# Optimization experiments

Hardware: AMD Instinct MI355X
Metric: run time of the kernel (lower is better)

The kernel has to match this reference:

```python
import jax, jax.numpy as jnp
import numpy as np

B, L, C = 256, 197, 768
H = C // 16          # reduction = 16
N_ADAPTERS = 10
EPS = 1e-12


def l2_normalize(x, axis=-1):
    sq = jnp.sum(x * x, axis=axis, keepdims=True)
    return x * jax.lax.rsqrt(jnp.maximum(sq, EPS))


def setup_inputs() -> dict:
    key = jax.random.key(0)
    k0, k1, k2, k3 = jax.random.split(key, 4)
    x_embed = jax.random.normal(k0, (B, L, C), dtype=jnp.float32)
    # torch nn.Linear weights are [out_features, in_features]
    W1 = jax.random.normal(k1, (N_ADAPTERS, H, C), dtype=jnp.float32) * 0.02
    W2 = jax.random.normal(k2, (N_ADAPTERS, C, H), dtype=jnp.float32) * 0.02
    adapter_key = jax.random.normal(k3, (N_ADAPTERS, C), dtype=jnp.float32)
    return {"x_embed": x_embed, "W1": W1, "W2": W2, "adapter_key": adapter_key}


def reference(x_embed, W1, W2, adapter_key):
    b = x_embed.shape[0]
    # embedding_key == 'mean'
    x_mean = jnp.mean(x_embed, axis=1)                 # [B, C]
    key_norm = l2_normalize(adapter_key, axis=1)       # [10, C]
    x_norm = l2_normalize(x_mean, axis=1)              # [B, C]
    similarity = x_norm @ key_norm.T                   # [B, 10]

    # top-1 per sample, then majority vote -> single adapter id for the whole batch.
    per_sample_idx = jnp.argmax(similarity, axis=1)    # [B]
    counts = jax.ops.segment_sum(jnp.ones((b,), jnp.float32), per_sample_idx,
                                 num_segments=N_ADAPTERS)
    major = jnp.argmax(counts)                         # ties -> smallest id, matching torch
    idx = jnp.full((b, 1), major, dtype=jnp.int32)     # out['adapter_idx']

    # Apply the selected adapter (same id for every sample); len(idx[i]) == 1.
    w1 = W1[major]                                     # [H, C]
    w2 = W2[major]                                     # [C, H]
    h = jax.nn.relu(jnp.einsum('blc,hc->blh', x_embed, w1))
    a = jax.nn.relu(jnp.einsum('blh,ch->blc', h, w2))
    bias = x_embed + a                                 # (x + adapter(x)) / 1

    adapter_norm = key_norm[idx]                       # [B, 1, C]
    reduce_sim = jnp.sum(adapter_norm * x_norm[:, None, :]) / b
    return bias, reduce_sim, idx
```

## Files before the change

### kernel.cpp

```cpp
#include <hip/hip_runtime.h>
#include <hip/hip_bf16.h>

#define B_   256
#define L_   197
#define C_   768
#define H_   48
#define NA_  10
#define ROWS (B_ * L_)
#define TR   16
#define XP   772
#define HP   72
#define NBLK (ROWS / TR)
#define OFF_SIM 38731776
#define OFF_IDX 38731777

typedef __attribute__((ext_vector_type(8))) short short8;
typedef __attribute__((ext_vector_type(4))) short short4_t;
typedef __attribute__((ext_vector_type(4))) float f32x4;

static __device__ inline short f2bf(float f) {
    union { float f; unsigned u; } v; v.f = f;
    unsigned r = v.u + 0x7fffu + ((v.u >> 16) & 1u);
    return (short)(r >> 16);
}

#define GL2LDS(g, l) __builtin_amdgcn_global_load_lds( \
    (const __attribute__((address_space(1))) void*)(g), \
    (__attribute__((address_space(3))) void*)(l), 16, 0, 0)

#define GLW(dst, p, OFF) asm volatile("global_load_dwordx4 %0, %1, off offset:" OFF \
    : "=v"(dst) : "v"(p))

__global__ void kw_convert(const float* __restrict__ W1, const float* __restrict__ W2,
                           short* __restrict__ W1b, short* __restrict__ W2b) {
    int i = blockIdx.x * 256 + threadIdx.x;
    if (i < NA_ * H_ * C_)
        W1b[i] = f2bf(W1[i]);
    if (i < NA_ * C_ * 64) {
        int k  = i & 63;
        int nc = i >> 6;
        W2b[i] = (k < H_) ? f2bf(W2[nc * H_ + k]) : (short)0;
    }
}

__global__ void k1a_partial(const float* __restrict__ x, float* __restrict__ partial) {
    int b = blockIdx.x >> 2, seg = blockIdx.x & 3;
    int l0 = seg * 50, l1 = l0 + 50; if (l1 > L_) l1 = L_;
    int t = threadIdx.x;
    const float* xb = x + (size_t)b * L_ * C_ + t * 4;
    float4 s = {0.f, 0.f, 0.f, 0.f};
    #pragma unroll 5
    for (int l = l0; l < l1; ++l) {
        float4 v = *(const float4*)(xb + (size_t)l * C_);
        s.x += v.x; s.y += v.y; s.z += v.z; s.w += v.w;
    }
    *(float4*)(partial + ((size_t)b * 4 + seg) * C_ + t * 4) = s;
}

__global__ void k1b_sims(const float* __restrict__ partial, const float* __restrict__ akey,
                         float* __restrict__ sims) {
    __shared__ float red[21][256];
    int b = blockIdx.x, t = threadIdx.x;
    const float* p = partial + (size_t)b * 4 * C_;
    float m[3];
    #pragma unroll
    for (int j = 0; j < 3; ++j) {
        int c = t + j * 256;
        m[j] = (p[c] + p[C_ + c] + p[2 * C_ + c] + p[3 * C_ + c]) * (1.f / (float)L_);
    }
    red[0][t] = m[0] * m[0] + m[1] * m[1] + m[2] * m[2];
    #pragma unroll
    for (int k = 0; k < NA_; ++k) {
        float kd = 0.f, kq = 0.f;
        #pragma unroll
        for (int j = 0; j < 3; ++j) {
            float kv = akey[k * C_ + t + j * 256];
            kd += m[j] * kv; kq += kv * kv;
        }
        red[1 + k][t] = kd; red[11 + k][t] = kq;
    }
    __syncthreads();
    for (int s = 128; s > 0; s >>= 1) {
        if (t < s) {
            #pragma unroll
            for (int q = 0; q < 21; ++q) red[q][t] += red[q][t + s];
        }
        __syncthreads();
    }
    if (t < NA_) {
        float msq = red[0][0];
        sims[b * NA_ + t] = red[1 + t][0] * rsqrtf(fmaxf(red[11 + t][0], 1e-12f))
                                          * rsqrtf(fmaxf(msq, 1e-12f));
    }
}

__global__ void k2_select(const float* __restrict__ sims, float* __restrict__ out,
                          int* __restrict__ majorp) {
    __shared__ int counts[NA_];
    __shared__ int majorS;
    __shared__ float rs[256];
    int t = threadIdx.x;
    float s[NA_];
    #pragma unroll
    for (int k = 0; k < NA_; ++k) s[k] = sims[t * NA_ + k];
    int best = 0; float bv = s[0];
    #pragma unroll
    for (int k = 1; k < NA_; ++k) { if (s[k] > bv) { bv = s[k]; best = k; } }
    if (t < NA_) counts[t] = 0;
    __syncthreads();
    atomicAdd(&counts[best], 1);
    __syncthreads();
    if (t == 0) {
        int mj = 0, mc = counts[0];
        #pragma unroll
        for (int k = 1; k < NA_; ++k) { if (counts[k] > mc) { mc = counts[k]; mj = k; } }
        majorS = mj; *majorp = mj;
    }
    __syncthreads();
    int mj = majorS;
    rs[t] = s[mj];
    __syncthreads();
    for (int st = 128; st > 0; st >>= 1) { if (t < st) rs[t] += rs[t + st]; __syncthreads(); }
    if (t == 0) out[OFF_SIM] = rs[0] * (1.f / (float)B_);
    out[OFF_IDX + t] = (float)mj;
}

__launch_bounds__(192, 2)
__global__ void k3_apply(const float* __restrict__ x, const short* __restrict__ W1b,
                         const short* __restrict__ W2b, const int* __restrict__ majorp,
                         float* __restrict__ out) {
    __shared__ float xs[TR * XP];
    __shared__ short hs[TR * HP];
    const int major = *majorp;

    int t = threadIdx.x;
    int w = t >> 6, l = t & 63;
    int rbase = blockIdx.x * TR;
    int lo16 = l & 15;
    int g = l >> 4;
    int klane = g * 8;

    {
        const float* xsrc = x + (size_t)rbase * C_ + w * 256 + l * 4;
        #pragma unroll
        for (int i = 0; i < TR; ++i)
            GL2LDS(xsrc + (size_t)i * C_, &xs[i * XP + w * 256]);
    }
    __syncthreads();

    {
        const short* w1p = W1b + major * (H_ * C_) + (size_t)(w * 16 + lo16) * C_ + klane;
        f32x4 acc = {0, 0, 0, 0};
        short8 q0, q1, q2, q3, q4, q5, q6, q7, q8, q9, q10, q11;

#define G1STEP(KK, Q) { \
        const int k0 = (KK) * 32; \
        f32x4 xa = *(const f32x4*)&xs[lo16 * XP + k0 + klane]; \
        f32x4 xb = *(const f32x4*)&xs[lo16 * XP + k0 + klane + 4]; \
        short8 af; \
        af[0] = f2bf(xa[0]); af[1] = f2bf(xa[1]); af[2] = f2bf(xa[2]); af[3] = f2bf(xa[3]); \
        af[4] = f2bf(xb[0]); af[5] = f2bf(xb[1]); af[6] = f2bf(xb[2]); af[7] = f2bf(xb[3]); \
        acc = __builtin_amdgcn_mfma_f32_16x16x32_bf16(af, Q, acc, 0, 0, 0); }

        GLW(q0, w1p, "0");    GLW(q1, w1p, "64");   GLW(q2, w1p, "128");
        GLW(q3, w1p, "192");  GLW(q4, w1p, "256");  GLW(q5, w1p, "320");
        GLW(q6, w1p, "384");  GLW(q7, w1p, "448");  GLW(q8, w1p, "512");
        GLW(q9, w1p, "576");  GLW(q10, w1p, "640"); GLW(q11, w1p, "704");
        asm volatile("s_waitcnt vmcnt(0)"
            : "+v"(q0), "+v"(q1), "+v"(q2), "+v"(q3), "+v"(q4), "+v"(q5),
              "+v"(q6), "+v"(q7), "+v"(q8), "+v"(q9), "+v"(q10), "+v"(q11));
        __builtin_amdgcn_sched_barrier(0);
        G1STEP(0, q0)  G1STEP(1, q1)  G1STEP(2, q2)  G1STEP(3, q3)
        G1STEP(4, q4)  G1STEP(5, q5)  G1STEP(6, q6)  G1STEP(7, q7)
        G1STEP(8, q8)  G1STEP(9, q9)  G1STEP(10, q10) G1STEP(11, q11)

        GLW(q0, w1p, "768");  GLW(q1, w1p, "832");  GLW(q2, w1p, "896");
        GLW(q3, w1p, "960");  GLW(q4, w1p, "1024"); GLW(q5, w1p, "1088");
        GLW(q6, w1p, "1152"); GLW(q7, w1p, "1216"); GLW(q8, w1p, "1280");
        GLW(q9, w1p, "1344"); GLW(q10, w1p, "1408"); GLW(q11, w1p, "1472");
        asm volatile("s_waitcnt vmcnt(0)"
            : "+v"(q0), "+v"(q1), "+v"(q2), "+v"(q3), "+v"(q4), "+v"(q5),
              "+v"(q6), "+v"(q7), "+v"(q8), "+v"(q9), "+v"(q10), "+v"(q11));
        __builtin_amdgcn_sched_barrier(0);
        G1STEP(12, q0) G1STEP(13, q1) G1STEP(14, q2) G1STEP(15, q3)
        G1STEP(16, q4) G1STEP(17, q5) G1STEP(18, q6) G1STEP(19, q7)
        G1STEP(20, q8) G1STEP(21, q9) G1STEP(22, q10) G1STEP(23, q11)
#undef G1STEP

        #pragma unroll
        for (int q = 0; q < 4; ++q)
            hs[(g * 4 + q) * HP + w * 16 + lo16] = f2bf(fmaxf(acc[q], 0.f));
        if (w == 0) {
            short4_t z = {0, 0, 0, 0};
            *(short4_t*)&hs[lo16 * HP + 48 + g * 4] = z;
        }
    }
    __syncthreads();

    {
        short8 hA = *(const short8*)&hs[lo16 * HP + klane];
        short8 hB = *(const short8*)&hs[lo16 * HP + 32 + klane];
        const short* w2base = W2b + (size_t)major * (C_ * 64) + lo16 * 64 + klane;

        #pragma unroll
        for (int b = 0; b < 4; ++b) {
            const int j0 = b * 4;
            const short* pa = w2base + (size_t)(w * 16 + j0) * 1024;
            const short* pb = pa + 2048;
            short8 r00, r01, r10, r11, r20, r21, r30, r31;
            GLW(r00, pa, "0");    GLW(r01, pa, "64");
            GLW(r10, pa, "2048"); GLW(r11, pa, "2112");
            GLW(r20, pb, "0");    GLW(r21, pb, "64");
            GLW(r30, pb, "2048"); GLW(r31, pb, "2112");
            asm volatile("s_waitcnt vmcnt(0)"
                : "+v"(r00), "+v"(r01), "+v"(r10), "+v"(r11),
                  "+v"(r20), "+v"(r21), "+v"(r30), "+v"(r31));
            __builtin_amdgcn_sched_barrier(0);

#define G2STEP(JJ, P0, P1) { \
            const int it = w * 16 + j0 + (JJ); \
            f32x4 acc = {0, 0, 0, 0}; \
            acc = __builtin_amdgcn_mfma_f32_16x16x32_bf16(P0, hA, acc, 0, 0, 0); \
            acc = __builtin_amdgcn_mfma_f32_16x16x32_bf16(P1, hB, acc, 0, 0, 0); \
            float* xp = &xs[lo16 * XP + it * 16 + g * 4]; \
            f32x4 xv = *(const f32x4*)xp; \
            f32x4 ov; \
            ov[0] = xv[0] + fmaxf(acc[0], 0.f); \
            ov[1] = xv[1] + fmaxf(acc[1], 0.f); \
            ov[2] = xv[2] + fmaxf(acc[2], 0.f); \
            ov[3] = xv[3] + fmaxf(acc[3], 0.f); \
            *(f32x4*)xp = ov; }

            G2STEP(0, r00, r01) G2STEP(1, r10, r11)
            G2STEP(2, r20, r21) G2STEP(3, r30, r31)
#undef G2STEP
        }
    }
    __syncthreads();

    {
        float* od = out + (size_t)rbase * C_ + t * 4;
        #pragma unroll
        for (int row = 0; row < TR; ++row) {
            f32x4 v = *(const f32x4*)&xs[row * XP + t * 4];
            *(f32x4*)(od + (size_t)row * C_) = v;
        }
    }
}

extern "C" void kernel_launch(void* const* d_in, const int* in_sizes, int n_in,
                              void* d_out, int out_size, void* d_ws, size_t ws_size,
                              hipStream_t stream) {
    const float* x    = (const float*)d_in[0];
    const float* W1   = (const float*)d_in[1];
    const float* W2   = (const float*)d_in[2];
    const float* akey = (const float*)d_in[3];
    float* out = (float*)d_out;

    char* ws = (char*)d_ws;
    short* W1b     = (short*)ws;
    short* W2b     = (short*)(ws + 737280);
    float* partial = (float*)(ws + 1720320);
    float* sims    = (float*)(ws + 4866048);
    int*   majorp  = (int*)(ws + 4876288);

    hipLaunchKernelGGL(kw_convert, dim3(1920), dim3(256), 0, stream, W1, W2, W1b, W2b);
    hipLaunchKernelGGL(k1a_partial, dim3(B_ * 4), dim3(192), 0, stream, x, partial);
    hipLaunchKernelGGL(k1b_sims, dim3(B_), dim3(256), 0, stream, partial, akey, sims);
    hipLaunchKernelGGL(k2_select, dim3(1), dim3(256), 0, stream, sims, out, majorp);
    hipLaunchKernelGGL(k3_apply, dim3(NBLK), dim3(192), 0, stream, x, W1b, W2b, majorp, out);
}
```

Measured before the change: 128.6 us.

## Prefetch all adapter weights up front and write outputs directly from registers

Issues all 24 W1 loads at once and waits on partial vmcnt counts, so the second half of the loads overlaps the first half of the MFMAs. W2 loads are likewise issued all at once, consumed in two waves, and the epilogue writes results straight to global memory. This removes the LDS round trip, the final barrier and the separate copy-out loop, and bf16 conversion now uses the HIP intrinsic. It raises register pressure, which may lower occupancy, and the direct stores are 16-byte scattered writes per lane rather than fully coalesced rows.

New measurement: 129.5 us. No clear change (+0.7%).

```diff
diff --git a/kernel.cpp b/kernel.cpp
--- a/kernel.cpp
+++ b/kernel.cpp
@@ -23,6 +23,11 @@
     unsigned r = v.u + 0x7fffu + ((v.u >> 16) & 1u);
     return (short)(r >> 16);
 }
+static __device__ inline short bfc(float f) {
+    __hip_bfloat16 h = __float2bfloat16(f);
+    union { __hip_bfloat16 h; short s; } u; u.h = h;
+    return u.s;
+}
 
 #define GL2LDS(g, l) __builtin_amdgcn_global_load_lds( \
     (const __attribute__((address_space(1))) void*)(g), \
@@ -152,44 +157,44 @@
         const short* w1p = W1b + major * (H_ * C_) + (size_t)(w * 16 + lo16) * C_ + klane;
         f32x4 acc = {0, 0, 0, 0};
         short8 q0, q1, q2, q3, q4, q5, q6, q7, q8, q9, q10, q11;
+        short8 q12, q13, q14, q15, q16, q17, q18, q19, q20, q21, q22, q23;
 
 #define G1STEP(KK, Q) { \
         const int k0 = (KK) * 32; \
         f32x4 xa = *(const f32x4*)&xs[lo16 * XP + k0 + klane]; \
         f32x4 xb = *(const f32x4*)&xs[lo16 * XP + k0 + klane + 4]; \
         short8 af; \
-        af[0] = f2bf(xa[0]); af[1] = f2bf(xa[1]); af[2] = f2bf(xa[2]); af[3] = f2bf(xa[3]); \
-        af[4] = f2bf(xb[0]); af[5] = f2bf(xb[1]); af[6] = f2bf(xb[2]); af[7] = f2bf(xb[3]); \
+        af[0] = bfc(xa[0]); af[1] = bfc(xa[1]); af[2] = bfc(xa[2]); af[3] = bfc(xa[3]); \
+        af[4] = bfc(xb[0]); af[5] = bfc(xb[1]); af[6] = bfc(xb[2]); af[7] = bfc(xb[3]); \
         acc = __builtin_amdgcn_mfma_f32_16x16x32_bf16(af, Q, acc, 0, 0, 0); }
 
-        GLW(q0, w1p, "0");    GLW(q1, w1p, "64");   GLW(q2, w1p, "128");
-        GLW(q3, w1p, "192");  GLW(q4, w1p, "256");  GLW(q5, w1p, "320");
-        GLW(q6, w1p, "384");  GLW(q7, w1p, "448");  GLW(q8, w1p, "512");
-        GLW(q9, w1p, "576");  GLW(q10, w1p, "640"); GLW(q11, w1p, "704");
-        asm volatile("s_waitcnt vmcnt(0)"
+        GLW(q0,  w1p, "0");    GLW(q1,  w1p, "64");   GLW(q2,  w1p, "128");
+        GLW(q3,  w1p, "192");  GLW(q4,  w1p, "256");  GLW(q5,  w1p, "320");
+        GLW(q6,  w1p, "384");  GLW(q7,  w1p, "448");  GLW(q8,  w1p, "512");
+        GLW(q9,  w1p, "576");  GLW(q10, w1p, "640");  GLW(q11, w1p, "704");
+        GLW(q12, w1p, "768");  GLW(q13, w1p, "832");  GLW(q14, w1p, "896");
+        GLW(q15, w1p, "960");  GLW(q16, w1p, "1024"); GLW(q17, w1p, "1088");
+        GLW(q18, w1p, "1152"); GLW(q19, w1p, "1216"); GLW(q20, w1p, "1280");
+        GLW(q21, w1p, "1344"); GLW(q22, w1p, "1408"); GLW(q23, w1p, "1472");
+        asm volatile("s_waitcnt vmcnt(12)"
             : "+v"(q0), "+v"(q1), "+v"(q2), "+v"(q3), "+v"(q4), "+v"(q5),
               "+v"(q6), "+v"(q7), "+v"(q8), "+v"(q9), "+v"(q10), "+v"(q11));
         __builtin_amdgcn_sched_barrier(0);
         G1STEP(0, q0)  G1STEP(1, q1)  G1STEP(2, q2)  G1STEP(3, q3)
         G1STEP(4, q4)  G1STEP(5, q5)  G1STEP(6, q6)  G1STEP(7, q7)
         G1STEP(8, q8)  G1STEP(9, q9)  G1STEP(10, q10) G1STEP(11, q11)
-
-        GLW(q0, w1p, "768");  GLW(q1, w1p, "832");  GLW(q2, w1p, "896");
-        GLW(q3, w1p, "960");  GLW(q4, w1p, "1024"); GLW(q5, w1p, "1088");
-        GLW(q6, w1p, "1152"); GLW(q7, w1p, "1216"); GLW(q8, w1p, "1280");
-        GLW(q9, w1p, "1344"); GLW(q10, w1p, "1408"); GLW(q11, w1p, "1472");
         asm volatile("s_waitcnt vmcnt(0)"
-            : "+v"(q0), "+v"(q1), "+v"(q2), "+v"(q3), "+v"(q4), "+v"(q5),
-              "+v"(q6), "+v"(q7), "+v"(q8), "+v"(q9), "+v"(q10), "+v"(q11));
-        __builtin_amdgcn_sched_barrier(0);
-        G1STEP(12, q0) G1STEP(13, q1) G1STEP(14, q2) G1STEP(15, q3)
-        G1STEP(16, q4) G1STEP(17, q5) G1STEP(18, q6) G1STEP(19, q7)
-        G1STEP(20, q8) G1STEP(21, q9) G1STEP(22, q10) G1STEP(23, q11)
+            : "+v"(q12), "+v"(q13), "+v"(q14), "+v"(q15), "+v"(q16), "+v"(q17),
+              "+v"(q18), "+v"(q19), "+v"(q20), "+v"(q21), "+v"(q22), "+v"(q23));
+        __builtin_amdgcn_sched_barrier(0);
+        G1STEP(12, q12) G1STEP(13, q13) G1STEP(14, q14) G1STEP(15, q15)
+        G1STEP(16, q16) G1STEP(17, q17) G1STEP(18, q18) G1STEP(19, q19)
+        G1STEP(20, q20) G1STEP(21, q21) G1STEP(22, q22) G1STEP(23, q23)
 #undef G1STEP
 
         #pragma unroll
         for (int q = 0; q < 4; ++q)
-            hs[(g * 4 + q) * HP + w * 16 + lo16] = f2bf(fmaxf(acc[q], 0.f));
+            hs[(g * 4 + q) * HP + w * 16 + lo16] = bfc(fmaxf(acc[q], 0.f));
         if (w == 0) {
             short4_t z = {0, 0, 0, 0};
             *(short4_t*)&hs[lo16 * HP + 48 + g * 4] = z;
@@ -200,51 +205,72 @@
     {
         short8 hA = *(const short8*)&hs[lo16 * HP + klane];
         short8 hB = *(const short8*)&hs[lo16 * HP + 32 + klane];
-        const short* w2base = W2b + (size_t)major * (C_ * 64) + lo16 * 64 + klane;
-
-        #pragma unroll
-        for (int b = 0; b < 4; ++b) {
-            const int j0 = b * 4;
-            const short* pa = w2base + (size_t)(w * 16 + j0) * 1024;
-            const short* pb = pa + 2048;
-            short8 r00, r01, r10, r11, r20, r21, r30, r31;
-            GLW(r00, pa, "0");    GLW(r01, pa, "64");
-            GLW(r10, pa, "2048"); GLW(r11, pa, "2112");
-            GLW(r20, pb, "0");    GLW(r21, pb, "64");
-            GLW(r30, pb, "2048"); GLW(r31, pb, "2112");
-            asm volatile("s_waitcnt vmcnt(0)"
-                : "+v"(r00), "+v"(r01), "+v"(r10), "+v"(r11),
-                  "+v"(r20), "+v"(r21), "+v"(r30), "+v"(r31));
-            __builtin_amdgcn_sched_barrier(0);
+        const short* ba = W2b + (size_t)major * (C_ * 64)
+                              + (size_t)(w * 16) * 1024 + lo16 * 64 + klane;
+        const short* b1 = ba + 2048;
+        const short* b2 = ba + 4096;
+        const short* b3 = ba + 6144;
+        const short* b4 = ba + 8192;
+        const short* b5 = ba + 10240;
+        const short* b6 = ba + 12288;
+        const short* b7 = ba + 14336;
+        short8 p0a, p0b, p1a, p1b, p2a, p2b, p3a, p3b;
+        short8 p4a, p4b, p5a, p5b, p6a, p6b, p7a, p7b;
+        short8 p8a, p8b, p9a, p9b, p10a, p10b, p11a, p11b;
+        short8 p12a, p12b, p13a, p13b, p14a, p14b, p15a, p15b;
+
+        GLW(p0a,  ba, "0");    GLW(p0b,  ba, "64");
+        GLW(p1a,  ba, "2048"); GLW(p1b,  ba, "2112");
+        GLW(p2a,  b1, "0");    GLW(p2b,  b1, "64");
+        GLW(p3a,  b1, "2048"); GLW(p3b,  b1, "2112");
+        GLW(p4a,  b2, "0");    GLW(p4b,  b2, "64");
+        GLW(p5a,  b2, "2048"); GLW(p5b,  b2, "2112");
+        GLW(p6a,  b3, "0");    GLW(p6b,  b3, "64");
+        GLW(p7a,  b3, "2048"); GLW(p7b,  b3, "2112");
+        GLW(p8a,  b4, "0");    GLW(p8b,  b4, "64");
+        GLW(p9a,  b4, "2048"); GLW(p9b,  b4, "2112");
+        GLW(p10a, b5, "0");    GLW(p10b, b5, "64");
+        GLW(p11a, b5, "2048"); GLW(p11b, b5, "2112");
+        GLW(p12a, b6, "0");    GLW(p12b, b6, "64");
+        GLW(p13a, b6, "2048"); GLW(p13b, b6, "2112");
+        GLW(p14a, b7, "0");    GLW(p14b, b7, "64");
+        GLW(p15a, b7, "2048"); GLW(p15b, b7, "2112");
+
+        float* outr = out + (size_t)(rbase + lo16) * C_ + w * 256 + g * 4;
 
 #define G2STEP(JJ, P0, P1) { \
-            const int it = w * 16 + j0 + (JJ); \
-            f32x4 acc = {0, 0, 0, 0}; \
-            acc = __builtin_amdgcn_mfma_f32_16x16x32_bf16(P0, hA, acc, 0, 0, 0); \
-            acc = __builtin_amdgcn_mfma_f32_16x16x32_bf16(P1, hB, acc, 0, 0, 0); \
-            float* xp = &xs[lo16 * XP + it * 16 + g * 4]; \
-            f32x4 xv = *(const f32x4*)xp; \
-            f32x4 ov; \
-            ov[0] = xv[0] + fmaxf(acc[0], 0.f); \
-            ov[1] = xv[1] + fmaxf(acc[1], 0.f); \
-            ov[2] = xv[2] + fmaxf(acc[2], 0.f); \
-            ov[3] = xv[3] + fmaxf(acc[3], 0.f); \
-            *(f32x4*)xp = ov; }
-
-            G2STEP(0, r00, r01) G2STEP(1, r10, r11)
-            G2STEP(2, r20, r21) G2STEP(3, r30, r31)
+        f32x4 acc = {0, 0, 0, 0}; \
+        acc = __builtin_amdgcn_mfma_f32_16x16x32_bf16(P0, hA, acc, 0, 0, 0); \
+        acc = __builtin_amdgcn_mfma_f32_16x16x32_bf16(P1, hB, acc, 0, 0, 0); \
+        const f32x4 xv = *(const f32x4*)&xs[lo16 * XP + (w * 16 + (JJ)) * 16 + g * 4]; \
+        f32x4 ov; \
+        ov[0] = xv[0] + fmaxf(acc[0], 0.f); \
+        ov[1] = xv[1] + fmaxf(acc[1], 0.f); \
+        ov[2] = xv[2] + fmaxf(acc[2], 0.f); \
+        ov[3] = xv[3] + fmaxf(acc[3], 0.f); \
+        *(f32x4*)(outr + (JJ) * 16) = ov; }
+
+        asm volatile("s_waitcnt vmcnt(16)"
+            : "+v"(p0a), "+v"(p0b), "+v"(p1a), "+v"(p1b),
+              "+v"(p2a), "+v"(p2b), "+v"(p3a), "+v"(p3b),
+              "+v"(p4a), "+v"(p4b), "+v"(p5a), "+v"(p5b),
+              "+v"(p6a), "+v"(p6b), "+v"(p7a), "+v"(p7b));
+        __builtin_amdgcn_sched_barrier(0);
+        G2STEP(0, p0a, p0b)   G2STEP(1, p1a, p1b)
+        G2STEP(2, p2a, p2b)   G2STEP(3, p3a, p3b)
+        G2STEP(4, p4a, p4b)   G2STEP(5, p5a, p5b)
+        G2STEP(6, p6a, p6b)   G2STEP(7, p7a, p7b)
+        asm volatile("s_waitcnt vmcnt(0)"
+            : "+v"(p8a), "+v"(p8b), "+v"(p9a), "+v"(p9b),
+              "+v"(p10a), "+v"(p10b), "+v"(p11a), "+v"(p11b),
+              "+v"(p12a), "+v"(p12b), "+v"(p13a), "+v"(p13b),
+              "+v"(p14a), "+v"(p14b), "+v"(p15a), "+v"(p15b));
+        __builtin_amdgcn_sched_barrier(0);
+        G2STEP(8, p8a, p8b)   G2STEP(9, p9a, p9b)
+        G2STEP(10, p10a, p10b) G2STEP(11, p11a, p11b)
+        G2STEP(12, p12a, p12b) G2STEP(13, p13a, p13b)
+        G2STEP(14, p14a, p14b) G2STEP(15, p15a, p15b)
 #undef G2STEP
-        }
-    }
-    __syncthreads();
-
-    {
-        float* od = out + (size_t)rbase * C_ + t * 4;
-        #pragma unroll
-        for (int row = 0; row < TR; ++row) {
-            f32x4 v = *(const f32x4*)&xs[row * XP + t * 4];
-            *(f32x4*)(od + (size_t)row * C_) = v;
-        }
     }
 }
 
```
